# Performance work log

Hardware: AMD Instinct MI355X
Metric: run time of the kernel (lower is better)

## Reference

```python
import jax, jax.numpy as jnp
import numpy as np

B, T, D = 2, 2048, 2048
N_HEADS, N_KV, HEAD_DIM = 16, 8, 128
SOFTCAP = 50.0
BIG_NEG = -2.3819763e38
ROPE_BASE = 10000.0


def apply_rope(x, positions):
    # x: [B, L, N, H], positions: [B, L]
    H = x.shape[-1]
    half = H // 2
    fraction = 2.0 * jnp.arange(half, dtype=jnp.float32) / H
    timescale = ROPE_BASE ** fraction  # [H/2]
    sinusoid = positions.astype(jnp.float32)[:, :, None, None] / timescale[None, None, None, :]  # [B,L,1,H/2]
    sin, cos = jnp.sin(sinusoid), jnp.cos(sinusoid)
    first, second = jnp.split(x, 2, axis=-1)
    out = jnp.concatenate([first * cos - second * sin, second * cos + first * sin], axis=-1)
    return out.astype(x.dtype)


def setup_inputs() -> dict:
    key = jax.random.key(0)
    k1, k2, k3, k4 = jax.random.split(key, 4)
    x = jax.random.normal(k1, (B, T, D), dtype=jnp.float32)
    positions = jnp.broadcast_to(jnp.arange(T, dtype=jnp.int32), (B, T))
    # causal mask [B, 1, T, S]
    attn_mask = jnp.broadcast_to(jnp.tril(jnp.ones((T, T), dtype=bool))[None, None], (B, 1, T, T))
    s = 1.0 / np.sqrt(D)
    w_q = jax.random.normal(k2, (N_HEADS, D, HEAD_DIM), dtype=jnp.float32) * s
    w_kv = jax.random.normal(k3, (2, N_KV, D, HEAD_DIM), dtype=jnp.float32) * s
    w_out = jax.random.normal(k4, (N_HEADS, HEAD_DIM, D), dtype=jnp.float32) * (1.0 / np.sqrt(N_HEADS * HEAD_DIM))
    return {"x": x, "positions": positions, "attn_mask": attn_mask, "w_q": w_q, "w_kv": w_kv, "w_out": w_out}


def reference(x, positions, attn_mask, w_q, w_kv, w_out):
    # projections (GQA branch: num_kv_heads != num_heads)
    q = jnp.einsum('btd,ndh->btnh', x, w_q)            # [B,T,N,H]
    kv = jnp.einsum('bsd,cndh->cbsnh', x, w_kv)        # [2,B,S,K,H]
    k, v = kv[0], kv[1]
    q = apply_rope(q, positions) * (HEAD_DIM ** -0.5)  # rsqrt_head_dim
    k = apply_rope(k, positions)
    G = N_HEADS // N_KV
    q = q.reshape(B, T, N_KV, G, HEAD_DIM)             # B T K G H
    logits = jnp.einsum('btkgh,bskh->bkgts', q, k).astype(jnp.float32)
    logits = jnp.tanh(logits / SOFTCAP) * SOFTCAP
    masked = jnp.where(attn_mask[:, :, None, :, :], logits, BIG_NEG)
    probs = jax.nn.softmax(masked, axis=-1).astype(k.dtype)
    encoded = jnp.einsum('bkgts,bskh->btkgh', probs, v).reshape(B, T, N_HEADS, HEAD_DIM)
    return jnp.einsum('btnh,nhd->btd', encoded, w_out)
```

## Files before the change

kernel.cpp:

```cpp
#include <hip/hip_runtime.h>


typedef unsigned short u16;
typedef __attribute__((ext_vector_type(8))) short short8;
typedef __attribute__((ext_vector_type(4))) float floatx4;

static __device__ __forceinline__ u16 f2b(float f){
  unsigned u = __float_as_uint(f);
  u = (u + 0x7fffu + ((u >> 16) & 1u)) >> 16;
  return (u16)u;
}
static __device__ __forceinline__ float b2f(u16 u){
  return __uint_as_float(((unsigned)u) << 16);
}
static __device__ __forceinline__ void gload16(const u16* g, u16* l){
  __builtin_amdgcn_global_load_lds(
      (const __attribute__((address_space(1))) unsigned int*)g,
      (__attribute__((address_space(3))) unsigned int*)l, 16, 0, 0);
}

__global__ void k_cvt_x(const float* __restrict__ x, u16* __restrict__ xb){
  int i = blockIdx.x * 256 + threadIdx.x;
  float4 v = ((const float4*)x)[i];
  ushort4 o = make_ushort4(f2b(v.x), f2b(v.y), f2b(v.z), f2b(v.w));
  ((ushort4*)xb)[i] = o;
}

__global__ void k_tr_f32(const float* __restrict__ src, u16* __restrict__ dst,
                         int sRS, int dRS, long sMS, long dMS){
  __shared__ float t[64][65];
  const float* s = src + (long)blockIdx.z * sMS + (long)blockIdx.y * 64 * sRS + (long)blockIdx.x * 64;
  u16* d = dst + (long)blockIdx.z * dMS + (long)blockIdx.x * 64 * dRS + (long)blockIdx.y * 64;
  int tid = threadIdx.x;
  #pragma unroll
  for(int i = 0; i < 16; i++){
    int idx = tid + 256 * i;
    t[idx >> 6][idx & 63] = s[(long)(idx >> 6) * sRS + (idx & 63)];
  }
  __syncthreads();
  #pragma unroll
  for(int i = 0; i < 16; i++){
    int idx = tid + 256 * i;
    d[(long)(idx >> 6) * dRS + (idx & 63)] = f2b(t[idx & 63][idx >> 6]);
  }
}

__global__ void k_tr_v(const u16* __restrict__ src, u16* __restrict__ dst){
  __shared__ u16 t[64][65];
  int z = blockIdx.z;
  const u16* s = src + ((long)(z >> 3) * 2048 + (long)blockIdx.y * 64) * 1024
                     + (z & 7) * 128 + blockIdx.x * 64;
  u16* d = dst + (long)z * 262144 + (long)blockIdx.x * 64 * 2048 + blockIdx.y * 64;
  int tid = threadIdx.x;
  #pragma unroll
  for(int i = 0; i < 16; i++){
    int idx = tid + 256 * i;
    t[idx >> 6][idx & 63] = s[(long)(idx >> 6) * 1024 + (idx & 63)];
  }
  __syncthreads();
  #pragma unroll
  for(int i = 0; i < 16; i++){
    int idx = tid + 256 * i;
    d[(long)(idx >> 6) * 2048 + (idx & 63)] = t[idx & 63][idx >> 6];
  }
}

__global__ __launch_bounds__(256) void k_gemm_qkv(
    const u16* __restrict__ A, const u16* __restrict__ wq_t, const u16* __restrict__ wkv_t,
    u16* __restrict__ qb, u16* __restrict__ kb, u16* __restrict__ vb){
  __shared__ __attribute__((aligned(16))) u16 sA[128 * 64];
  __shared__ __attribute__((aligned(16))) u16 sB[128 * 64];
  int mt = blockIdx.x, nt = blockIdx.y;
  const u16* Bt; u16* dst; int dS, dcol;
  if(nt < 16){ Bt = wq_t + (long)nt * 262144; dst = qb; dS = 2048; dcol = nt * 128; }
  else {
    Bt = wkv_t + (long)(nt - 16) * 262144;
    dS = 1024;
    if(nt < 24){ dst = kb; dcol = (nt - 16) * 128; }
    else       { dst = vb; dcol = (nt - 24) * 128; }
  }
  int tid = threadIdx.x;
  int lane = tid & 63, wave = tid >> 6, l15 = lane & 15, quad = lane >> 4;
  int ro = (wave & 1) * 64, co = (wave >> 1) * 64;
  int xm7 = l15 & 7;
  int srow = tid >> 3;
  int gch  = (tid & 7) ^ (srow & 7);
  const u16* Ag = A  + ((long)(mt * 128) + srow) * 2048 + (gch << 3);
  const u16* Bg = Bt + (long)srow * 2048 + (gch << 3);
  u16* lA = sA + tid * 8;
  u16* lB = sB + tid * 8;
  floatx4 acc[4][4];
  const floatx4 fz = {0.f, 0.f, 0.f, 0.f};
  #pragma unroll
  for(int r = 0; r < 4; r++)
    #pragma unroll
    for(int c = 0; c < 4; c++) acc[r][c] = fz;
  for(int k0 = 0; k0 < 2048; k0 += 64){
    #pragma unroll
    for(int r = 0; r < 4; r++){
      gload16(Ag + (long)r * 65536 + k0, lA + r * 2048);
      gload16(Bg + (long)r * 65536 + k0, lB + r * 2048);
    }
    __syncthreads();
    #pragma unroll
    for(int ks = 0; ks < 2; ks++){
      short8 af[4], bfr[4];
      #pragma unroll
      for(int r = 0; r < 4; r++)
        af[r]  = *(const short8*)(sA + ((ro + r * 16 + l15) << 6) + ((((ks << 2) | quad) ^ xm7) << 3));
      #pragma unroll
      for(int c = 0; c < 4; c++)
        bfr[c] = *(const short8*)(sB + ((co + c * 16 + l15) << 6) + ((((ks << 2) | quad) ^ xm7) << 3));
      #pragma unroll
      for(int r = 0; r < 4; r++)
        #pragma unroll
        for(int c = 0; c < 4; c++)
          acc[r][c] = __builtin_amdgcn_mfma_f32_16x16x32_bf16(af[r], bfr[c], acc[r][c], 0, 0, 0);
    }
    __syncthreads();
  }
  long rb0 = (long)mt * 128 + ro + quad * 4;
  #pragma unroll
  for(int r = 0; r < 4; r++)
    #pragma unroll
    for(int c = 0; c < 4; c++){
      int col = dcol + co + c * 16 + l15;
      #pragma unroll
      for(int j = 0; j < 4; j++)
        dst[(rb0 + r * 16 + j) * dS + col] = f2b(acc[r][c][j]);
    }
}

__global__ __launch_bounds__(256) void k_gemm_out(
    const u16* __restrict__ A, const u16* __restrict__ Bt0, float* __restrict__ C){
  __shared__ __attribute__((aligned(16))) u16 sA[128 * 64];
  __shared__ __attribute__((aligned(16))) u16 sB[128 * 64];
  int mt = blockIdx.x, nt = blockIdx.y;
  const u16* Bt = Bt0 + (long)nt * 262144;
  int tid = threadIdx.x;
  int lane = tid & 63, wave = tid >> 6, l15 = lane & 15, quad = lane >> 4;
  int ro = (wave & 1) * 64, co = (wave >> 1) * 64;
  int xm7 = l15 & 7;
  int srow = tid >> 3;
  int gch  = (tid & 7) ^ (srow & 7);
  const u16* Ag = A  + ((long)(mt * 128) + srow) * 2048 + (gch << 3);
  const u16* Bg = Bt + (long)srow * 2048 + (gch << 3);
  u16* lA = sA + tid * 8;
  u16* lB = sB + tid * 8;
  floatx4 acc[4][4];
  const floatx4 fz = {0.f, 0.f, 0.f, 0.f};
  #pragma unroll
  for(int r = 0; r < 4; r++)
    #pragma unroll
    for(int c = 0; c < 4; c++) acc[r][c] = fz;
  for(int k0 = 0; k0 < 2048; k0 += 64){
    #pragma unroll
    for(int r = 0; r < 4; r++){
      gload16(Ag + (long)r * 65536 + k0, lA + r * 2048);
      gload16(Bg + (long)r * 65536 + k0, lB + r * 2048);
    }
    __syncthreads();
    #pragma unroll
    for(int ks = 0; ks < 2; ks++){
      short8 af[4], bfr[4];
      #pragma unroll
      for(int r = 0; r < 4; r++)
        af[r]  = *(const short8*)(sA + ((ro + r * 16 + l15) << 6) + ((((ks << 2) | quad) ^ xm7) << 3));
      #pragma unroll
      for(int c = 0; c < 4; c++)
        bfr[c] = *(const short8*)(sB + ((co + c * 16 + l15) << 6) + ((((ks << 2) | quad) ^ xm7) << 3));
      #pragma unroll
      for(int r = 0; r < 4; r++)
        #pragma unroll
        for(int c = 0; c < 4; c++)
          acc[r][c] = __builtin_amdgcn_mfma_f32_16x16x32_bf16(af[r], bfr[c], acc[r][c], 0, 0, 0);
    }
    __syncthreads();
  }
  long rb0 = (long)mt * 128 + ro + quad * 4;
  #pragma unroll
  for(int r = 0; r < 4; r++)
    #pragma unroll
    for(int c = 0; c < 4; c++){
      int col = nt * 128 + co + c * 16 + l15;
      #pragma unroll
      for(int j = 0; j < 4; j++)
        C[(rb0 + r * 16 + j) * 2048 + col] = acc[r][c][j];
    }
}

__global__ void k_sincos(const int* __restrict__ pos, float* __restrict__ tab){
  int idx = blockIdx.x * 256 + threadIdx.x;
  int row = idx >> 6, h = idx & 63;
  float pf = (float)pos[row];
  float inv = exp2f(-0.20762050593045077f * (float)h);
  float ang = pf * inv;
  tab[(row << 7) + h]      = sinf(ang);
  tab[(row << 7) + 64 + h] = cosf(ang);
}

__global__ void k_rope(u16* __restrict__ qb, u16* __restrict__ kb,
                       const float* __restrict__ tab){
  int idx = blockIdx.x * 256 + threadIdx.x;
  const int NQ = 4096 * 16 * 64;
  u16* p1; int row, h; float scale;
  if(idx < NQ){
    row = idx >> 10;
    int rr = idx & 1023;
    int n = rr >> 6; h = rr & 63;
    p1 = qb + (long)row * 2048 + n * 128 + h;
    scale = 0.08838834764831845f;
  } else {
    int j = idx - NQ;
    row = j >> 9;
    int rr = j & 511;
    int n = rr >> 6; h = rr & 63;
    p1 = kb + (long)row * 1024 + n * 128 + h;
    scale = 1.0f;
  }
  float sv = tab[(row << 7) + h], cv = tab[(row << 7) + 64 + h];
  float x1 = b2f(p1[0]), x2 = b2f(p1[64]);
  float o1 = (x1 * cv - x2 * sv) * scale;
  float o2 = (x2 * cv + x1 * sv) * scale;
  p1[0] = f2b(o1); p1[64] = f2b(o2);
}

__global__ __launch_bounds__(256) void k_flash(
    const u16* __restrict__ qb, const u16* __restrict__ kb,
    const u16* __restrict__ vt, u16* __restrict__ enc){
  __shared__ __attribute__((aligned(16))) u16 sK[2 * 64 * 128];
  __shared__ __attribute__((aligned(16))) u16 sVt[2 * 128 * 64];
  __shared__ __attribute__((aligned(16))) u16 sP[4][16][72];
  int qt = 31 - blockIdx.y;
  int hidx = blockIdx.x;
  int b = hidx >> 4, kv = (hidx >> 1) & 7, g = hidx & 1;
  int tid = threadIdx.x;
  int lane = tid & 63, wave = tid >> 6, l15 = lane & 15, quad = lane >> 4;

  short8 qf[4];
  {
    const u16* qg = qb + ((long)b * 2048 + qt * 64 + wave * 16 + l15) * 2048
                       + (kv * 2 + g) * 128 + quad * 8;
    #pragma unroll
    for(int ks = 0; ks < 4; ks++) qf[ks] = *(const short8*)(qg + ks * 32);
  }

  int krow = tid >> 4;
  int kch  = (tid & 15) ^ krow;
  const u16* Kg = kb + ((long)b * 2048 + krow) * 1024 + kv * 128 + (kch << 3);
  int vrow = tid >> 3;
  int vch  = (tid & 7) ^ (vrow & 7);
  const u16* Vg = vt + ((long)(b * 8 + kv) * 128 + vrow) * 2048 + (vch << 3);
  u16* lK = sK  + tid * 8;
  u16* lV = sVt + tid * 8;
  #pragma unroll
  for(int r = 0; r < 4; r++){
    gload16(Kg + (long)r * 16384, lK + r * 2048);
    gload16(Vg + (long)r * 65536, lV + r * 2048);
  }

  float l_loc[4] = {0.f, 0.f, 0.f, 0.f};
  floatx4 o_acc[8];
  const floatx4 fz = {0.f, 0.f, 0.f, 0.f};
  #pragma unroll
  for(int c = 0; c < 8; c++) o_acc[c] = fz;

  const float c1 = 0.057707801635558536f;
  const float c2 = -144.26950408889634f;
  const float c3 = 72.13475204444817f;

  for(int kt = 0; kt <= qt; kt++){
    int buf = (kt & 1) * 8192;
    __syncthreads();
    if(kt < qt){
      int nb = buf ^ 8192;
      #pragma unroll
      for(int r = 0; r < 4; r++){
        gload16(Kg + (long)(kt + 1) * 65536 + (long)r * 16384, lK + nb + r * 2048);
        gload16(Vg + (kt + 1) * 64 + (long)r * 65536, lV + nb + r * 2048);
      }
    }
    floatx4 s_acc[4];
    #pragma unroll
    for(int c = 0; c < 4; c++) s_acc[c] = fz;
    #pragma unroll
    for(int ks = 0; ks < 4; ks++){
      #pragma unroll
      for(int cb = 0; cb < 4; cb++){
        short8 bk = *(const short8*)(sK + buf + ((cb * 16 + l15) << 7)
                                     + ((((ks << 2) | quad) ^ l15) << 3));
        s_acc[cb] = __builtin_amdgcn_mfma_f32_16x16x32_bf16(qf[ks], bk, s_acc[cb], 0, 0, 0);
      }
    }
    bool diag = (kt == qt);
    int rloc = wave * 16 + quad * 4;
    #pragma unroll
    for(int r = 0; r < 4; r++){
      #pragma unroll
      for(int cb = 0; cb < 4; cb++){
        float s = s_acc[cb][r];
        float u = __builtin_amdgcn_exp2f(c1 * s);
        float d = __builtin_amdgcn_rcpf(u + 1.f);
        float p = __builtin_amdgcn_exp2f(__builtin_fmaf(c2, d, c3));
        if(diag && (cb * 16 + l15 > rloc + r)) p = 0.f;
        l_loc[r] += p;
        sP[wave][quad * 4 + r][cb * 16 + l15] = f2b(p);
      }
    }
    #pragma unroll
    for(int ks2 = 0; ks2 < 2; ks2++){
      short8 ap = *(const short8*)&sP[wave][l15][ks2 * 32 + quad * 8];
      #pragma unroll
      for(int c = 0; c < 8; c++){
        short8 bv = *(const short8*)(sVt + buf + ((c * 16 + l15) << 6)
                                     + ((((ks2 << 2) | quad) ^ (l15 & 7)) << 3));
        o_acc[c] = __builtin_amdgcn_mfma_f32_16x16x32_bf16(ap, bv, o_acc[c], 0, 0, 0);
      }
    }
  }
  #pragma unroll
  for(int r = 0; r < 4; r++){
    float l = l_loc[r];
    #pragma unroll
    for(int off = 1; off < 16; off <<= 1) l += __shfl_xor(l, off);
    float invl = 1.f / l;
    long rowe = (long)b * 2048 + qt * 64 + wave * 16 + quad * 4 + r;
    #pragma unroll
    for(int c = 0; c < 8; c++)
      enc[rowe * 2048 + (kv * 2 + g) * 128 + c * 16 + l15] = f2b(o_acc[c][r] * invl);
  }
}

extern "C" void kernel_launch(void* const* d_in, const int* in_sizes, int n_in,
                              void* d_out, int out_size, void* d_ws, size_t ws_size,
                              hipStream_t stream){
  const float* x     = (const float*)d_in[0];
  const int*   posi  = (const int*)  d_in[1];
  const float* w_q   = (const float*)d_in[3];
  const float* w_kv  = (const float*)d_in[4];
  const float* w_out = (const float*)d_in[5];
  float* out = (float*)d_out;

  char* w = (char*)d_ws;
  u16* xb     = (u16*)(w);
  u16* wq_t   = (u16*)(w + 16777216);
  u16* wkv_t  = (u16*)(w + 25165824);
  u16* wout_t = (u16*)(w + 33554432);
  u16* q_buf  = (u16*)(w + 41943040);
  u16* k_buf  = (u16*)(w + 58720256);
  u16* v_buf  = (u16*)(w + 67108864);
  u16* v_t    = (u16*)(w + 75497472);
  float* tab  = (float*)(w);
  u16* enc    = xb;

  k_cvt_x   <<<8192, 256, 0, stream>>>(x, xb);
  k_tr_f32  <<<dim3(2, 32, 16), 256, 0, stream>>>(w_q,   wq_t,   128, 2048, 262144L, 262144L);
  k_tr_f32  <<<dim3(2, 32, 16), 256, 0, stream>>>(w_kv,  wkv_t,  128, 2048, 262144L, 262144L);
  k_tr_f32  <<<dim3(32, 32, 1), 256, 0, stream>>>(w_out, wout_t, 2048, 2048, 0L, 0L);
  k_gemm_qkv<<<dim3(32, 32), 256, 0, stream>>>(xb, wq_t, wkv_t, q_buf, k_buf, v_buf);
  k_sincos  <<<1024, 256, 0, stream>>>(posi, tab);
  k_rope    <<<24576, 256, 0, stream>>>(q_buf, k_buf, tab);
  k_tr_v    <<<dim3(2, 32, 16), 256, 0, stream>>>(v_buf, v_t);
  k_flash   <<<dim3(32, 32), 256, 0, stream>>>(q_buf, k_buf, v_t, enc);
  k_gemm_out<<<dim3(32, 16), 256, 0, stream>>>(enc, wout_t, out);
}
```

Before: 356.0 us.

## Fuse prep kernels and move RoPE and V transpose into QKV GEMM epilogue

Merges the x conversion, three weight transposes and the sin/cos table into one prep launch. The QKV GEMM now stages its tile in shared memory and applies RoPE and the query scale before writing Q and K, and writes V directly in transposed layout. This removes the separate rope and V-transpose kernels and their extra global round trips. The flash kernel also splits off-diagonal tiles from the masked diagonal tile so the mask check only runs on the diagonal. In exchange, the GEMM epilogue gains an extra shared-memory pass and a barrier.

```diff
diff --git a/kernel.cpp b/kernel.cpp
--- a/kernel.cpp
+++ b/kernel.cpp
@@ -19,19 +19,8 @@
       (__attribute__((address_space(3))) unsigned int*)l, 16, 0, 0);
 }
 
-__global__ void k_cvt_x(const float* __restrict__ x, u16* __restrict__ xb){
-  int i = blockIdx.x * 256 + threadIdx.x;
-  float4 v = ((const float4*)x)[i];
-  ushort4 o = make_ushort4(f2b(v.x), f2b(v.y), f2b(v.z), f2b(v.w));
-  ((ushort4*)xb)[i] = o;
-}
-
-__global__ void k_tr_f32(const float* __restrict__ src, u16* __restrict__ dst,
-                         int sRS, int dRS, long sMS, long dMS){
-  __shared__ float t[64][65];
-  const float* s = src + (long)blockIdx.z * sMS + (long)blockIdx.y * 64 * sRS + (long)blockIdx.x * 64;
-  u16* d = dst + (long)blockIdx.z * dMS + (long)blockIdx.x * 64 * dRS + (long)blockIdx.y * 64;
-  int tid = threadIdx.x;
+static __device__ void tr64(const float* __restrict__ s, u16* __restrict__ d,
+                            int sRS, int dRS, float (*t)[65], int tid){
   #pragma unroll
   for(int i = 0; i < 16; i++){
     int idx = tid + 256 * i;
@@ -45,40 +34,55 @@
   }
 }
 
-__global__ void k_tr_v(const u16* __restrict__ src, u16* __restrict__ dst){
-  __shared__ u16 t[64][65];
-  int z = blockIdx.z;
-  const u16* s = src + ((long)(z >> 3) * 2048 + (long)blockIdx.y * 64) * 1024
-                     + (z & 7) * 128 + blockIdx.x * 64;
-  u16* d = dst + (long)z * 262144 + (long)blockIdx.x * 64 * 2048 + blockIdx.y * 64;
-  int tid = threadIdx.x;
-  #pragma unroll
-  for(int i = 0; i < 16; i++){
-    int idx = tid + 256 * i;
-    t[idx >> 6][idx & 63] = s[(long)(idx >> 6) * 1024 + (idx & 63)];
-  }
-  __syncthreads();
-  #pragma unroll
-  for(int i = 0; i < 16; i++){
-    int idx = tid + 256 * i;
-    d[(long)(idx >> 6) * 2048 + (idx & 63)] = t[idx & 63][idx >> 6];
+__global__ __launch_bounds__(256) void k_prep(
+    const float* __restrict__ x, u16* __restrict__ xb,
+    const float* __restrict__ wq, u16* __restrict__ wq_t,
+    const float* __restrict__ wkv, u16* __restrict__ wkv_t,
+    const float* __restrict__ wo, u16* __restrict__ wo_t,
+    const int* __restrict__ pos, float* __restrict__ tab){
+  __shared__ float t[64][65];
+  int blk = blockIdx.x, tid = threadIdx.x;
+  if(blk < 8192){
+    int i = blk * 256 + tid;
+    float4 v = ((const float4*)x)[i];
+    ushort4 o = make_ushort4(f2b(v.x), f2b(v.y), f2b(v.z), f2b(v.w));
+    ((ushort4*)xb)[i] = o;
+  } else if(blk < 9216){
+    int q = blk - 8192;
+    int bx = q & 1, by = (q >> 1) & 31, bz = q >> 6;
+    tr64(wq + (long)bz * 262144 + (long)by * 64 * 128 + bx * 64,
+         wq_t + (long)bz * 262144 + (long)bx * 64 * 2048 + by * 64, 128, 2048, t, tid);
+  } else if(blk < 10240){
+    int q = blk - 9216;
+    int bx = q & 1, by = (q >> 1) & 31, bz = q >> 6;
+    tr64(wkv + (long)bz * 262144 + (long)by * 64 * 128 + bx * 64,
+         wkv_t + (long)bz * 262144 + (long)bx * 64 * 2048 + by * 64, 128, 2048, t, tid);
+  } else if(blk < 11264){
+    int q = blk - 10240;
+    int bx = q & 31, by = q >> 5;
+    tr64(wo + (long)by * 64 * 2048 + bx * 64,
+         wo_t + (long)bx * 64 * 2048 + by * 64, 2048, 2048, t, tid);
+  } else {
+    int idx = (blk - 11264) * 256 + tid;
+    int row = idx >> 6, h = idx & 63;
+    float pf = (float)pos[row];
+    float inv = exp2f(-0.20762050593045077f * (float)h);
+    float ang = pf * inv;
+    tab[(row << 7) + h]      = sinf(ang);
+    tab[(row << 7) + 64 + h] = cosf(ang);
   }
 }
 
 __global__ __launch_bounds__(256) void k_gemm_qkv(
     const u16* __restrict__ A, const u16* __restrict__ wq_t, const u16* __restrict__ wkv_t,
-    u16* __restrict__ qb, u16* __restrict__ kb, u16* __restrict__ vb){
-  __shared__ __attribute__((aligned(16))) u16 sA[128 * 64];
-  __shared__ __attribute__((aligned(16))) u16 sB[128 * 64];
+    const float* __restrict__ tab,
+    u16* __restrict__ qb, u16* __restrict__ kb, u16* __restrict__ vtp){
+  __shared__ __attribute__((aligned(16))) u16 pool[128 * 132];
+  u16* sA = pool;
+  u16* sB = pool + 8192;
   int mt = blockIdx.x, nt = blockIdx.y;
-  const u16* Bt; u16* dst; int dS, dcol;
-  if(nt < 16){ Bt = wq_t + (long)nt * 262144; dst = qb; dS = 2048; dcol = nt * 128; }
-  else {
-    Bt = wkv_t + (long)(nt - 16) * 262144;
-    dS = 1024;
-    if(nt < 24){ dst = kb; dcol = (nt - 16) * 128; }
-    else       { dst = vb; dcol = (nt - 24) * 128; }
-  }
+  const u16* Bt = (nt < 16) ? (wq_t + (long)nt * 262144)
+                            : (wkv_t + (long)(nt - 16) * 262144);
   int tid = threadIdx.x;
   int lane = tid & 63, wave = tid >> 6, l15 = lane & 15, quad = lane >> 4;
   int ro = (wave & 1) * 64, co = (wave >> 1) * 64;
@@ -119,16 +123,55 @@
     }
     __syncthreads();
   }
-  long rb0 = (long)mt * 128 + ro + quad * 4;
+  u16* sT = pool;
   #pragma unroll
   for(int r = 0; r < 4; r++)
     #pragma unroll
     for(int c = 0; c < 4; c++){
-      int col = dcol + co + c * 16 + l15;
-      #pragma unroll
-      for(int j = 0; j < 4; j++)
-        dst[(rb0 + r * 16 + j) * dS + col] = f2b(acc[r][c][j]);
-    }
+      int row = ro + r * 16 + quad * 4, col = co + c * 16 + l15;
+      #pragma unroll
+      for(int j = 0; j < 4; j++) sT[(row + j) * 132 + col] = f2b(acc[r][c][j]);
+    }
+  __syncthreads();
+  int grow0 = mt * 128;
+  if(nt < 24){
+    float scale = (nt < 16) ? 0.08838834764831845f : 1.0f;
+    u16* dst = (nt < 16) ? qb : kb;
+    int dS   = (nt < 16) ? 2048 : 1024;
+    int dcol = (nt < 16) ? nt * 128 : (nt - 16) * 128;
+    #pragma unroll
+    for(int it = 0; it < 16; it++){
+      int idx = tid + 256 * it;
+      int row = idx >> 5, cw = idx & 31;
+      int grow = grow0 + row;
+      unsigned lo = *(const unsigned*)&sT[row * 132 + 2 * cw];
+      unsigned hi = *(const unsigned*)&sT[row * 132 + 64 + 2 * cw];
+      float2 sn = *(const float2*)&tab[(grow << 7) + 2 * cw];
+      float2 cs = *(const float2*)&tab[(grow << 7) + 64 + 2 * cw];
+      float x1a = b2f((u16)lo), x1b = b2f((u16)(lo >> 16));
+      float x2a = b2f((u16)hi), x2b = b2f((u16)(hi >> 16));
+      float o1a = (x1a * cs.x - x2a * sn.x) * scale;
+      float o1b = (x1b * cs.y - x2b * sn.y) * scale;
+      float o2a = (x2a * cs.x + x1a * sn.x) * scale;
+      float o2b = (x2b * cs.y + x1b * sn.y) * scale;
+      unsigned w1 = (unsigned)f2b(o1a) | ((unsigned)f2b(o1b) << 16);
+      unsigned w2 = (unsigned)f2b(o2a) | ((unsigned)f2b(o2b) << 16);
+      *(unsigned*)&dst[(long)grow * dS + dcol + 2 * cw] = w1;
+      *(unsigned*)&dst[(long)grow * dS + dcol + 64 + 2 * cw] = w2;
+    }
+  } else {
+    int b = mt >> 4, kvh = nt - 24;
+    u16* vt = vtp + (long)(b * 8 + kvh) * 262144;
+    int tcol0 = (mt & 15) * 128;
+    int h = tid >> 1, s0 = (tid & 1) * 64;
+    #pragma unroll
+    for(int i = 0; i < 16; i++){
+      int s = s0 + i * 4;
+      ushort4 v4 = make_ushort4(sT[(s    ) * 132 + h], sT[(s + 1) * 132 + h],
+                                sT[(s + 2) * 132 + h], sT[(s + 3) * 132 + h]);
+      *(ushort4*)&vt[(long)h * 2048 + tcol0 + s] = v4;
+    }
+  }
 }
 
 __global__ __launch_bounds__(256) void k_gemm_out(
@@ -189,42 +232,6 @@
     }
 }
 
-__global__ void k_sincos(const int* __restrict__ pos, float* __restrict__ tab){
-  int idx = blockIdx.x * 256 + threadIdx.x;
-  int row = idx >> 6, h = idx & 63;
-  float pf = (float)pos[row];
-  float inv = exp2f(-0.20762050593045077f * (float)h);
-  float ang = pf * inv;
-  tab[(row << 7) + h]      = sinf(ang);
-  tab[(row << 7) + 64 + h] = cosf(ang);
-}
-
-__global__ void k_rope(u16* __restrict__ qb, u16* __restrict__ kb,
-                       const float* __restrict__ tab){
-  int idx = blockIdx.x * 256 + threadIdx.x;
-  const int NQ = 4096 * 16 * 64;
-  u16* p1; int row, h; float scale;
-  if(idx < NQ){
-    row = idx >> 10;
-    int rr = idx & 1023;
-    int n = rr >> 6; h = rr & 63;
-    p1 = qb + (long)row * 2048 + n * 128 + h;
-    scale = 0.08838834764831845f;
-  } else {
-    int j = idx - NQ;
-    row = j >> 9;
-    int rr = j & 511;
-    int n = rr >> 6; h = rr & 63;
-    p1 = kb + (long)row * 1024 + n * 128 + h;
-    scale = 1.0f;
-  }
-  float sv = tab[(row << 7) + h], cv = tab[(row << 7) + 64 + h];
-  float x1 = b2f(p1[0]), x2 = b2f(p1[64]);
-  float o1 = (x1 * cv - x2 * sv) * scale;
-  float o2 = (x2 * cv + x1 * sv) * scale;
-  p1[0] = f2b(o1); p1[64] = f2b(o2);
-}
-
 __global__ __launch_bounds__(256) void k_flash(
     const u16* __restrict__ qb, const u16* __restrict__ kb,
     const u16* __restrict__ vt, u16* __restrict__ enc){
@@ -292,19 +299,33 @@
         s_acc[cb] = __builtin_amdgcn_mfma_f32_16x16x32_bf16(qf[ks], bk, s_acc[cb], 0, 0, 0);
       }
     }
-    bool diag = (kt == qt);
-    int rloc = wave * 16 + quad * 4;
-    #pragma unroll
-    for(int r = 0; r < 4; r++){
-      #pragma unroll
-      for(int cb = 0; cb < 4; cb++){
-        float s = s_acc[cb][r];
-        float u = __builtin_amdgcn_exp2f(c1 * s);
-        float d = __builtin_amdgcn_rcpf(u + 1.f);
-        float p = __builtin_amdgcn_exp2f(__builtin_fmaf(c2, d, c3));
-        if(diag && (cb * 16 + l15 > rloc + r)) p = 0.f;
-        l_loc[r] += p;
-        sP[wave][quad * 4 + r][cb * 16 + l15] = f2b(p);
+    if(kt < qt){
+      #pragma unroll
+      for(int r = 0; r < 4; r++){
+        #pragma unroll
+        for(int cb = 0; cb < 4; cb++){
+          float s = s_acc[cb][r];
+          float u = __builtin_amdgcn_exp2f(c1 * s);
+          float d = __builtin_amdgcn_rcpf(u + 1.f);
+          float p = __builtin_amdgcn_exp2f(__builtin_fmaf(c2, d, c3));
+          l_loc[r] += p;
+          sP[wave][quad * 4 + r][cb * 16 + l15] = f2b(p);
+        }
+      }
+    } else {
+      int rloc = wave * 16 + quad * 4;
+      #pragma unroll
+      for(int r = 0; r < 4; r++){
+        #pragma unroll
+        for(int cb = 0; cb < 4; cb++){
+          float s = s_acc[cb][r];
+          float u = __builtin_amdgcn_exp2f(c1 * s);
+          float d = __builtin_amdgcn_rcpf(u + 1.f);
+          float p = __builtin_amdgcn_exp2f(__builtin_fmaf(c2, d, c3));
+          if(cb * 16 + l15 > rloc + r) p = 0.f;
+          l_loc[r] += p;
+          sP[wave][quad * 4 + r][cb * 16 + l15] = f2b(p);
+        }
       }
     }
     #pragma unroll
@@ -348,19 +369,12 @@
   u16* wout_t = (u16*)(w + 33554432);
   u16* q_buf  = (u16*)(w + 41943040);
   u16* k_buf  = (u16*)(w + 58720256);
-  u16* v_buf  = (u16*)(w + 67108864);
-  u16* v_t    = (u16*)(w + 75497472);
-  float* tab  = (float*)(w);
+  u16* v_t    = (u16*)(w + 67108864);
+  float* tab  = (float*)(w + 75497472);
   u16* enc    = xb;
 
-  k_cvt_x   <<<8192, 256, 0, stream>>>(x, xb);
-  k_tr_f32  <<<dim3(2, 32, 16), 256, 0, stream>>>(w_q,   wq_t,   128, 2048, 262144L, 262144L);
-  k_tr_f32  <<<dim3(2, 32, 16), 256, 0, stream>>>(w_kv,  wkv_t,  128, 2048, 262144L, 262144L);
-  k_tr_f32  <<<dim3(32, 32, 1), 256, 0, stream>>>(w_out, wout_t, 2048, 2048, 0L, 0L);
-  k_gemm_qkv<<<dim3(32, 32), 256, 0, stream>>>(xb, wq_t, wkv_t, q_buf, k_buf, v_buf);
-  k_sincos  <<<1024, 256, 0, stream>>>(posi, tab);
-  k_rope    <<<24576, 256, 0, stream>>>(q_buf, k_buf, tab);
-  k_tr_v    <<<dim3(2, 32, 16), 256, 0, stream>>>(v_buf, v_t);
+  k_prep    <<<12288, 256, 0, stream>>>(x, xb, w_q, wq_t, w_kv, wkv_t, w_out, wout_t, posi, tab);
+  k_gemm_qkv<<<dim3(32, 32), 256, 0, stream>>>(xb, wq_t, wkv_t, tab, q_buf, k_buf, v_t);
   k_flash   <<<dim3(32, 32), 256, 0, stream>>>(q_buf, k_buf, v_t, enc);
   k_gemm_out<<<dim3(32, 16), 256, 0, stream>>>(enc, wout_t, out);
 }
```

After: 333.0 us. 1.07x faster.
